# Kernel optimization log

Hardware: AMD Instinct MI355X
Metric: run time of the kernel (lower is better)

The kernel has to match this reference:

```python
import jax, jax.numpy as jnp
import numpy as np

DIM = 64; LAYERS = 3; NREL = 8; NB = 4
NNODE = 150000; NEDGE = 1000000; NSEDGE = 200000
BATCH = 1024; SEQ = 20; NPRED = 20; NITEM = 100000
TD = 2 * LAYERS * DIM  # 384
NEG = np.float32(-(2 ** 32) + 1)


def rgcn_layer(x, src, dst, et, basis, comp, root, bias):
    # basis decomposition: W_r = sum_b comp[r,b] * basis[b]  -> [R,d,d]
    W = jnp.einsum('rb,bde->rde', comp, basis)
    # transform all nodes by every relation once, then gather per edge
    xw = jnp.einsum('nd,rde->rne', x, W)          # [R,N,d]
    msgs = xw[et, src]                            # [E,d] gather (rate==1 gating)
    agg = jax.ops.segment_sum(msgs, dst, num_segments=x.shape[0])
    return agg + x @ root + bias


def tsal(seq, WQ, WK, WV):
    # hand-rolled causal self-attention, head_num=1; NOTE: softmax over axis=1
    # (query axis), faithful to F.softmax(output_tensor, 1) in the source.
    T = seq.shape[1]
    Q = seq @ WQ; K = seq @ WK; V = seq @ WV
    scores = jnp.einsum('bid,bjd->bij', Q, K) / jnp.sqrt(jnp.float32(T))
    tril = jnp.tril(jnp.ones((T, T), dtype=scores.dtype))
    scores = jnp.where(tril == 0, NEG, scores)
    attn = jax.nn.softmax(scores, axis=1)
    return jnp.einsum('bij,bjd->bid', attn, V)


def setup_inputs() -> dict:
    key = jax.random.key(0)
    ks = jax.random.split(key, 24)
    xav = lambda k, sh: jax.random.uniform(k, sh, jnp.float32, -1.0, 1.0) * np.float32(np.sqrt(6.0 / (sh[-1] + sh[-2])))
    node_emb = (jax.random.normal(ks[0], (NNODE, DIM), jnp.float32) / DIM).at[0].set(0.0)
    predict_w = (jax.random.normal(ks[1], (NITEM, TD), jnp.float32) / TD).at[0].set(0.0)
    predict_b = jnp.zeros((NITEM, 1), jnp.float32)
    sc_w = np.float32(np.sqrt(1.0 / DIM))
    basis = jax.random.normal(ks[2], (LAYERS, NB, DIM, DIM), jnp.float32) * sc_w
    comp = jax.random.normal(ks[3], (LAYERS, NREL, NB), jnp.float32) * np.float32(1.0 / NB)
    root = jax.random.normal(ks[4], (LAYERS, DIM, DIM), jnp.float32) * sc_w
    bias = jnp.zeros((LAYERS, DIM), jnp.float32)
    sbasis = jax.random.normal(ks[5], (LAYERS, NB, DIM, DIM), jnp.float32) * sc_w
    scomp = jax.random.normal(ks[6], (LAYERS, NREL, NB), jnp.float32) * np.float32(1.0 / NB)
    sroot = jax.random.normal(ks[7], (LAYERS, DIM, DIM), jnp.float32) * sc_w
    sbias = jnp.zeros((LAYERS, DIM), jnp.float32)
    WQ = xav(ks[8], (TD, TD)); WK = xav(ks[9], (TD, TD)); WV = xav(ks[10], (TD, TD))
    batch_users = jax.random.randint(ks[11], (BATCH,), 0, NNODE)
    batch_sequences = jax.random.randint(ks[12], (BATCH, SEQ), 0, NNODE)
    items_to_predict = jax.random.randint(ks[13], (BATCH, NPRED), 0, NITEM)
    edge_index = jax.random.randint(ks[14], (2, NEDGE), 0, NNODE)
    edge_type = jax.random.randint(ks[15], (NEDGE,), 0, NREL)
    node_no = jnp.arange(NNODE)
    short_edge_index = jax.random.randint(ks[16], (2, NSEDGE), 0, NNODE)
    short_edge_type = jax.random.randint(ks[17], (NSEDGE,), 0, NREL)
    return {"node_emb": node_emb, "predict_w": predict_w, "predict_b": predict_b,
            "basis": basis, "comp": comp, "root": root, "bias": bias,
            "sbasis": sbasis, "scomp": scomp, "sroot": sroot, "sbias": sbias,
            "WQ": WQ, "WK": WK, "WV": WV,
            "batch_users": batch_users, "batch_sequences": batch_sequences,
            "items_to_predict": items_to_predict, "edge_index": edge_index,
            "edge_type": edge_type, "node_no": node_no,
            "short_edge_index": short_edge_index, "short_edge_type": short_edge_type}


def reference(node_emb, predict_w, predict_b, basis, comp, root, bias,
              sbasis, scomp, sroot, sbias, WQ, WK, WV,
              batch_users, batch_sequences, items_to_predict,
              edge_index, edge_type, node_no, short_edge_index, short_edge_type):
    x = node_emb[node_no]
    states = []
    for l in range(LAYERS):
        x = jnp.tanh(rgcn_layer(x, edge_index[0], edge_index[1], edge_type,
                                basis[l], comp[l], root[l], bias[l]))
        states.append(x)
    for l in range(LAYERS):
        x = jnp.tanh(rgcn_layer(x, short_edge_index[0], short_edge_index[1], short_edge_type,
                                sbasis[l], scomp[l], sroot[l], sbias[l]))
        states.append(x)
    cs = jnp.concatenate(states, axis=1)             # [N, 2*LAYERS*DIM]
    user_emb = cs[batch_users]                       # [B, TD]
    item_embs_conv = cs[batch_sequences]             # [B, L, TD]
    item_embs = tsal(item_embs_conv, WQ, WK, WV)     # [B, L, TD]
    pe_w = predict_w[items_to_predict]               # [B, K, TD]
    pe_b = predict_b[items_to_predict][..., 0]       # [B, K]
    res = jnp.einsum('bkd,bd->bk', pe_w, user_emb) + pe_b      # baddbmm
    res = res + jnp.einsum('bld,bkd->bk', item_embs, pe_w)     # rel_score summed over L
    return (res, user_emb, item_embs_conv)
```

## Files before the change

kernel.cpp:

```cpp
#include <hip/hip_runtime.h>
#include <hip/hip_fp16.h>

typedef unsigned short u16;
typedef unsigned int   u32;

#define DIM    64
#define NREL   8
#define NB     4
#define NNODE  150000
#define NEDGE  1000000
#define NSEDGE 200000
#define BATCH  1024
#define SEQL   20
#define NPRED  20
#define TD     384

#define KC     576
#define KH     1152
#define KTILES 36
#define ROWD   580
#define NODES_PER_TILE 16

#define SCAN_CHUNK 2048

typedef float    f32x4 __attribute__((ext_vector_type(4)));
typedef _Float16 f16x8 __attribute__((ext_vector_type(8)));

__device__ __forceinline__ u32 packsplit(float v) {
    __half h = __float2half_rn(v);
    __half l = __float2half_rn(v - __half2float(h));
    __half2 p; p.x = h; p.y = l;
    u32 r;
    __builtin_memcpy(&r, &p, 4);
    return r;
}

__global__ __launch_bounds__(256) void wpackf_kernel(const float* __restrict__ comp,
                                                     const float* __restrict__ basis,
                                                     const float* __restrict__ root,
                                                     u32* __restrict__ Wf) {
    int idx = blockIdx.x * 256 + threadIdx.x;
    if (idx >= KTILES * 4 * 64) return;
    int l  = idx & 63;
    int f  = idx >> 6;
    int kt = f >> 2, ct = f & 3;
    int j  = ct * 16 + (l & 15);
    int kb = kt * 32 + (l >> 4) * 8;
    union { f16x8 v; u16 h[8]; } out;
#pragma unroll
    for (int u = 0; u < 8; ++u) {
        int c = (kb + u) >> 1;
        float v;
        if (c < 512) {
            int r = c >> 6, d = c & 63;
            v = comp[r * NB + 0] * basis[0 * 4096 + d * 64 + j]
              + comp[r * NB + 1] * basis[1 * 4096 + d * 64 + j]
              + comp[r * NB + 2] * basis[2 * 4096 + d * 64 + j]
              + comp[r * NB + 3] * basis[3 * 4096 + d * 64 + j];
        } else {
            int d = c & 63;
            v = root[d * 64 + j];
        }
        out.h[u] = (u16)__half_as_ushort(__float2half_rn(v));
    }
    *((f16x8*)Wf + idx) = out.v;
}


__global__ __launch_bounds__(256) void hist_kernel(const int* __restrict__ dst,
                                                   const int* __restrict__ typ,
                                                   int* __restrict__ cnt8, int E) {
    int i = blockIdx.x * 256 + threadIdx.x;
    const int stride = gridDim.x * 256;
    for (; i < E; i += stride) atomicAdd(&cnt8[dst[i] * NREL + typ[i]], 1);
}

__global__ __launch_bounds__(256) void blocksum_kernel(const int* __restrict__ cnt,
                                                       int* __restrict__ bsum, int N) {
    const int base = blockIdx.x * SCAN_CHUNK + threadIdx.x * 8;
    int s = 0;
#pragma unroll
    for (int u = 0; u < 8; ++u) {
        const int i = base + u;
        s += (i < N) ? cnt[i] : 0;
    }
#pragma unroll
    for (int o = 1; o < 64; o <<= 1) s += __shfl_xor(s, o, 64);
    __shared__ int ws[4];
    if ((threadIdx.x & 63) == 0) ws[threadIdx.x >> 6] = s;
    __syncthreads();
    if (threadIdx.x == 0) bsum[blockIdx.x] = ws[0] + ws[1] + ws[2] + ws[3];
}

__global__ __launch_bounds__(1024) void scanbsum_kernel(int* __restrict__ bsum, int B) {
    __shared__ int sh[1024];
    const int t = threadIdx.x;
    const int v = (t < B) ? bsum[t] : 0;
    sh[t] = v;
    __syncthreads();
    for (int o = 1; o < 1024; o <<= 1) {
        const int u = (t >= o) ? sh[t - o] : 0;
        __syncthreads();
        sh[t] += u;
        __syncthreads();
    }
    if (t < B) bsum[t] = sh[t] - v;
}

__global__ __launch_bounds__(256) void alloc2_kernel(const int* __restrict__ cnt,
                                                     const int* __restrict__ bsum,
                                                     int* __restrict__ rstart,
                                                     int* __restrict__ cursor, int N) {
    const int base = blockIdx.x * SCAN_CHUNK + threadIdx.x * 8;
    const int lane = threadIdx.x & 63;
    int c[8];
    int s = 0;
#pragma unroll
    for (int u = 0; u < 8; ++u) {
        const int i = base + u;
        c[u] = (i < N) ? cnt[i] : 0;
        s += c[u];
    }
    int v = s;
#pragma unroll
    for (int o = 1; o < 64; o <<= 1) {
        const int u2 = __shfl_up(v, o, 64);
        if (lane >= o) v += u2;
    }
    __shared__ int ws[4];
    if (lane == 63) ws[threadIdx.x >> 6] = v;
    __syncthreads();
    const int wv = threadIdx.x >> 6;
    int waveoff = 0;
#pragma unroll
    for (int k = 0; k < 4; ++k) waveoff += (k < wv) ? ws[k] : 0;
    int tbase = bsum[blockIdx.x] + waveoff + (v - s);
#pragma unroll
    for (int u = 0; u < 8; ++u) {
        const int i = base + u;
        if (i < N) {
            rstart[i] = tbase;
            cursor[i] = tbase;
            tbase += c[u];
        }
    }
}

__global__ __launch_bounds__(256) void scatter_kernel(const int* __restrict__ src,
                                                      const int* __restrict__ dst,
                                                      const int* __restrict__ typ,
                                                      int* __restrict__ cursor8,
                                                      u32* __restrict__ psrc, int E) {
    int i = blockIdx.x * 256 + threadIdx.x;
    const int stride = gridDim.x * 256;
    for (; i < E; i += stride) {
        const int slot = atomicAdd(&cursor8[dst[i] * NREL + typ[i]], 1);
        psrc[slot] = (u32)src[i];
    }
}

__global__ __launch_bounds__(512) void rgcn_mfma_kernel(const float* __restrict__ x,
                                                        const u32* __restrict__ Wf,
                                                        const float* __restrict__ bias,
                                                        const int* __restrict__ starts8,
                                                        const int* __restrict__ ends8,
                                                        const u32* __restrict__ psrc,
                                                        float* __restrict__ xout, int N) {
    __shared__ u32 Xl[NODES_PER_TILE * ROWD];
    const int lane = threadIdx.x & 63;
    const int w = threadIdx.x >> 6;
    const int NT = (N + NODES_PER_TILE - 1) / NODES_PER_TILE;
    const int l15 = lane & 15, g = lane >> 4;

    for (int tile = blockIdx.x; tile < NT; tile += gridDim.x) {
        const int base = tile * NODES_PER_TILE;
        for (int u = 0; u < 2; ++u) {
            const int row = w * 2 + u;
            const int n = base + row;
            if (n < N) {
                u32* Xrow = Xl + row * ROWD;
                const float xn = x[(size_t)n * 64 + lane];
                const int stl = starts8[n * NREL + (lane & 7)];
                const int enl = ends8[n * NREL + (lane & 7)];
                const int st0 = __shfl(stl, 0, 64);
                const int en7 = __shfl(enl, 7, 64);
                if (en7 - st0 <= 64) {
                    const u32 pk = (lane < en7 - st0) ? psrc[st0 + lane] : 0u;
#pragma unroll
                    for (int r = 0; r < NREL; ++r) {
                        const int st = __shfl(stl, r, 64) - st0;
                        const int en = __shfl(enl, r, 64) - st0;
                        float a0 = 0.f, a1 = 0.f;
                        int i = st;
                        for (; i + 1 < en; i += 2) {
                            const int s0 = (int)__shfl((int)pk, i, 64);
                            const int s1 = (int)__shfl((int)pk, i + 1, 64);
                            a0 += x[(size_t)s0 * 64 + lane];
                            a1 += x[(size_t)s1 * 64 + lane];
                        }
                        if (i < en) {
                            const int s0 = (int)__shfl((int)pk, i, 64);
                            a0 += x[(size_t)s0 * 64 + lane];
                        }
                        Xrow[r * 64 + lane] = packsplit(a0 + a1);
                    }
                } else {
#pragma unroll 1
                    for (int r = 0; r < NREL; ++r) {
                        const int st = __shfl(stl, r, 64);
                        const int en = __shfl(enl, r, 64);
                        float acc = 0.f;
                        for (int i2 = st; i2 < en; i2 += 64) {
                            int mm = en - i2; if (mm > 64) mm = 64;
                            int pkc = (lane < mm) ? (int)psrc[i2 + lane] : 0;
                            for (int t = 0; t < mm; ++t) {
                                const int s = __shfl(pkc, t, 64);
                                acc += x[(size_t)s * 64 + lane];
                            }
                        }
                        Xrow[r * 64 + lane] = packsplit(acc);
                    }
                }
                Xrow[512 + lane] = packsplit(xn);
            }
        }
        __syncthreads();
        if (w < 4) {
            const int ct = w;
            const u32* Arow = Xl + l15 * ROWD + g * 4;
            const f16x8* Bf = (const f16x8*)Wf + ct * 64 + lane;
            f32x4 acc = {0.f, 0.f, 0.f, 0.f};
#pragma unroll 4
            for (int kt = 0; kt < KTILES; ++kt) {
                f16x8 a = *(const f16x8*)(Arow + kt * 16);
                f16x8 b = Bf[kt * 256];
                acc = __builtin_amdgcn_mfma_f32_16x16x32_f16(a, b, acc, 0, 0, 0);
            }
            const int col = ct * 16 + l15;
            const float bc = bias[col];
#pragma unroll
            for (int q = 0; q < 4; ++q) {
                const int n = base + g * 4 + q;
                if (n < N) xout[(size_t)n * 64 + col] = tanhf(acc[q] + bc);
            }
        }
        __syncthreads();
    }
}

__global__ __launch_bounds__(256) void post_kernel(const float* __restrict__ xc,
                                                   const int* __restrict__ users,
                                                   const int* __restrict__ seqs,
                                                   float* __restrict__ msum,
                                                   float* __restrict__ out_user,
                                                   float* __restrict__ out_seq, int l) {
    const int lane = threadIdx.x & 63;
    int wave = blockIdx.x * 4 + (threadIdx.x >> 6);
    const int nw = gridDim.x * 4;
    for (int p = wave; p < BATCH * SEQL; p += nw) {
        const int idx = seqs[p];
        out_seq[(size_t)p * TD + l * 64 + lane] = xc[(size_t)idx * 64 + lane];
    }
    for (int b = wave; b < BATCH; b += nw) {
        out_user[(size_t)b * TD + l * 64 + lane] = xc[(size_t)users[b] * 64 + lane];
        float m = 0.f;
        for (int t = 0; t < SEQL; ++t)
            m += xc[(size_t)seqs[b * SEQL + t] * 64 + lane];
        msum[(size_t)b * TD + l * 64 + lane] = m;
    }
}

__global__ __launch_bounds__(384) void final_kernel(const float* __restrict__ msum,
                                                    const float* __restrict__ user_f32,
                                                    const float* __restrict__ WV,
                                                    const float* __restrict__ pw,
                                                    const float* __restrict__ pb,
                                                    const int* __restrict__ items,
                                                    float* __restrict__ out_res) {
    __shared__ float ms[TD];
    __shared__ float uL[TD];
    const int b = blockIdx.x;
    const int o = threadIdx.x;
    ms[o] = msum[(size_t)b * TD + o];
    __syncthreads();
    float sv = 0.f;
#pragma unroll 4
    for (int d = 0; d < TD; ++d) sv += ms[d] * WV[d * TD + o];
    uL[o] = user_f32[(size_t)b * TD + o] + sv;
    __syncthreads();
    const int w = threadIdx.x >> 6, lane = threadIdx.x & 63;
    for (int k = w; k < NPRED; k += 6) {
        const int item = items[b * NPRED + k];
        const float* pwr = pw + (size_t)item * TD;
        float a = 0.f;
#pragma unroll
        for (int d = lane; d < TD; d += 64) a += pwr[d] * uL[d];
#pragma unroll
        for (int off = 32; off; off >>= 1) a += __shfl_down(a, off, 64);
        if (lane == 0) out_res[b * NPRED + k] = a + pb[item];
    }
}

extern "C" void kernel_launch(void* const* d_in, const int* in_sizes, int n_in,
                              void* d_out, int out_size, void* d_ws, size_t ws_size,
                              hipStream_t stream) {
    const float* node_emb  = (const float*)d_in[0];
    const float* predict_w = (const float*)d_in[1];
    const float* predict_b = (const float*)d_in[2];
    const float* basis     = (const float*)d_in[3];
    const float* comp      = (const float*)d_in[4];
    const float* root      = (const float*)d_in[5];
    const float* bias      = (const float*)d_in[6];
    const float* sbasis    = (const float*)d_in[7];
    const float* scomp     = (const float*)d_in[8];
    const float* sroot     = (const float*)d_in[9];
    const float* sbias     = (const float*)d_in[10];
    const float* WV        = (const float*)d_in[13];
    const int* users       = (const int*)d_in[14];
    const int* seqs        = (const int*)d_in[15];
    const int* items       = (const int*)d_in[16];
    const int* eidx        = (const int*)d_in[17];
    const int* etyp        = (const int*)d_in[18];
    const int* seidx       = (const int*)d_in[20];
    const int* setyp       = (const int*)d_in[21];

    float* xA    = (float*)d_ws;
    float* xB    = xA + (size_t)NNODE * 64;
    u32*   Wf    = (u32*)(xB + (size_t)NNODE * 64);
    float* msum  = (float*)(Wf + KTILES * 4 * 64 * 4);
    int*   cnt8  = (int*)(msum + (size_t)BATCH * TD);
    int*   stB   = cnt8 + (size_t)NNODE * NREL;
    int*   enB   = stB  + (size_t)NNODE * NREL;
    int*   stS   = enB  + (size_t)NNODE * NREL;
    int*   enS   = stS  + (size_t)NNODE * NREL;
    int*   bsum  = enS  + (size_t)NNODE * NREL;
    u32*   pB    = (u32*)(bsum + 1024);
    u32*   pS    = pB + NEDGE;

    float* out      = (float*)d_out;
    float* out_res  = out;
    float* out_user = out + BATCH * NPRED;
    float* out_seq  = out_user + (size_t)BATCH * TD;

    const int N8 = NNODE * NREL;
    const int NBLK = (N8 + SCAN_CHUNK - 1) / SCAN_CHUNK;
    hipMemsetAsync(cnt8, 0, (size_t)N8 * sizeof(int), stream);
    hist_kernel<<<2048, 256, 0, stream>>>(eidx + NEDGE, etyp, cnt8, NEDGE);
    blocksum_kernel<<<NBLK, 256, 0, stream>>>(cnt8, bsum, N8);
    scanbsum_kernel<<<1, 1024, 0, stream>>>(bsum, NBLK);
    alloc2_kernel<<<NBLK, 256, 0, stream>>>(cnt8, bsum, stB, enB, N8);
    scatter_kernel<<<2048, 256, 0, stream>>>(eidx, eidx + NEDGE, etyp, enB, pB, NEDGE);
    hipMemsetAsync(cnt8, 0, (size_t)N8 * sizeof(int), stream);
    hist_kernel<<<784, 256, 0, stream>>>(seidx + NSEDGE, setyp, cnt8, NSEDGE);
    blocksum_kernel<<<NBLK, 256, 0, stream>>>(cnt8, bsum, N8);
    scanbsum_kernel<<<1, 1024, 0, stream>>>(bsum, NBLK);
    alloc2_kernel<<<NBLK, 256, 0, stream>>>(cnt8, bsum, stS, enS, N8);
    scatter_kernel<<<784, 256, 0, stream>>>(seidx, seidx + NSEDGE, setyp, enS, pS, NSEDGE);

    const float* xc = node_emb;
    for (int l = 0; l < 6; ++l) {
        const float *bs, *cp, *rt, *bi;
        const int *rs, *re;
        const u32* pk;
        if (l < 3) {
            bs = basis  + (size_t)l * NB * DIM * DIM;
            cp = comp   + l * NREL * NB;
            rt = root   + l * DIM * DIM;
            bi = bias   + l * DIM;
            rs = stB; re = enB; pk = pB;
        } else {
            const int m = l - 3;
            bs = sbasis + (size_t)m * NB * DIM * DIM;
            cp = scomp  + m * NREL * NB;
            rt = sroot  + m * DIM * DIM;
            bi = sbias  + m * DIM;
            rs = stS; re = enS; pk = pS;
        }
        float* xg = (l & 1) ? xB : xA;
        wpackf_kernel<<<36, 256, 0, stream>>>(cp, bs, rt, Wf);
        rgcn_mfma_kernel<<<2048, 512, 0, stream>>>(xc, Wf, bi, rs, re, pk, xg, NNODE);
        post_kernel<<<320, 256, 0, stream>>>(xg, users, seqs, msum, out_user, out_seq, l);
        xc = xg;
    }

    final_kernel<<<BATCH, 384, 0, stream>>>(msum, out_user, WV, predict_w, predict_b,
                                            items, out_res);
}
```

Measured before the change: 1.169 ms.

## Pack relation type into edge source index and accumulate per-relation in LDS

The scatter kernel now stores the edge type in the upper bits of each packed source index. The aggregation loop can then walk all of a node's edges in one flat pass, four gathers at a time, and add each row into a per-relation float slot in shared memory instead of running eight separate per-relation loops. Per-node metadata, self features and the first 64 packed indices for both nodes are loaded up front to overlap the latency. In exchange, accumulation goes through LDS read-modify-write, and the packing assumes node ids fit in 18 bits.

```diff
diff --git a/kernel.cpp b/kernel.cpp
--- a/kernel.cpp
+++ b/kernel.cpp
@@ -155,7 +155,7 @@
     const int stride = gridDim.x * 256;
     for (; i < E; i += stride) {
         const int slot = atomicAdd(&cursor8[dst[i] * NREL + typ[i]], 1);
-        psrc[slot] = (u32)src[i];
+        psrc[slot] = (u32)src[i] | ((u32)typ[i] << 18);
     }
 }
 
@@ -174,54 +174,69 @@
 
     for (int tile = blockIdx.x; tile < NT; tile += gridDim.x) {
         const int base = tile * NODES_PER_TILE;
+        const int n0 = base + w * 2;
+        int nst0 = 0, nen0 = 0, nst1 = 0, nen1 = 0;
+        float xn0 = 0.f, xn1 = 0.f;
+        if (n0 < N) {
+            nst0 = starts8[n0 * NREL];
+            nen0 = ends8[n0 * NREL + 7];
+            xn0  = x[(size_t)n0 * 64 + lane];
+        }
+        if (n0 + 1 < N) {
+            nst1 = starts8[(n0 + 1) * NREL];
+            nen1 = ends8[(n0 + 1) * NREL + 7];
+            xn1  = x[(size_t)(n0 + 1) * 64 + lane];
+        }
+        u32 pk0 = 0, pk1 = 0;
+        if (lane < nen0 - nst0) pk0 = psrc[nst0 + lane];
+        if (lane < nen1 - nst1) pk1 = psrc[nst1 + lane];
+#pragma unroll
         for (int u = 0; u < 2; ++u) {
-            const int row = w * 2 + u;
-            const int n = base + row;
+            const int n = n0 + u;
             if (n < N) {
+                const int row = w * 2 + u;
                 u32* Xrow = Xl + row * ROWD;
-                const float xn = x[(size_t)n * 64 + lane];
-                const int stl = starts8[n * NREL + (lane & 7)];
-                const int enl = ends8[n * NREL + (lane & 7)];
-                const int st0 = __shfl(stl, 0, 64);
-                const int en7 = __shfl(enl, 7, 64);
-                if (en7 - st0 <= 64) {
-                    const u32 pk = (lane < en7 - st0) ? psrc[st0 + lane] : 0u;
-#pragma unroll
-                    for (int r = 0; r < NREL; ++r) {
-                        const int st = __shfl(stl, r, 64) - st0;
-                        const int en = __shfl(enl, r, 64) - st0;
-                        float a0 = 0.f, a1 = 0.f;
-                        int i = st;
-                        for (; i + 1 < en; i += 2) {
-                            const int s0 = (int)__shfl((int)pk, i, 64);
-                            const int s1 = (int)__shfl((int)pk, i + 1, 64);
-                            a0 += x[(size_t)s0 * 64 + lane];
-                            a1 += x[(size_t)s1 * 64 + lane];
+                float* XrowF = (float*)Xrow;
+#pragma unroll
+                for (int r = 0; r < NREL; ++r) XrowF[r * 64 + lane] = 0.f;
+                const u32 pk = u ? pk1 : pk0;
+                const int nst = u ? nst1 : nst0;
+                const int nen = u ? nen1 : nen0;
+                const int tot = nen - nst;
+                const int cw = tot > 64 ? 64 : tot;
+                int t = 0;
+                for (; t + 4 <= cw; t += 4) {
+                    const u32 p0 = __shfl(pk, t + 0, 64);
+                    const u32 p1 = __shfl(pk, t + 1, 64);
+                    const u32 p2 = __shfl(pk, t + 2, 64);
+                    const u32 p3 = __shfl(pk, t + 3, 64);
+                    const float v0 = x[(size_t)(p0 & 0x3FFFFu) * 64 + lane];
+                    const float v1 = x[(size_t)(p1 & 0x3FFFFu) * 64 + lane];
+                    const float v2 = x[(size_t)(p2 & 0x3FFFFu) * 64 + lane];
+                    const float v3 = x[(size_t)(p3 & 0x3FFFFu) * 64 + lane];
+                    XrowF[(p0 >> 18) * 64 + lane] += v0;
+                    XrowF[(p1 >> 18) * 64 + lane] += v1;
+                    XrowF[(p2 >> 18) * 64 + lane] += v2;
+                    XrowF[(p3 >> 18) * 64 + lane] += v3;
+                }
+                for (; t < cw; ++t) {
+                    const u32 p = __shfl(pk, t, 64);
+                    XrowF[(p >> 18) * 64 + lane] += x[(size_t)(p & 0x3FFFFu) * 64 + lane];
+                }
+                if (tot > 64) {
+                    for (int i2 = nst + 64; i2 < nen; i2 += 64) {
+                        int mm = nen - i2; if (mm > 64) mm = 64;
+                        const u32 pkc = (lane < mm) ? psrc[i2 + lane] : 0u;
+                        for (int tt = 0; tt < mm; ++tt) {
+                            const u32 p = __shfl(pkc, tt, 64);
+                            XrowF[(p >> 18) * 64 + lane] += x[(size_t)(p & 0x3FFFFu) * 64 + lane];
                         }
-                        if (i < en) {
-                            const int s0 = (int)__shfl((int)pk, i, 64);
-                            a0 += x[(size_t)s0 * 64 + lane];
-                        }
-                        Xrow[r * 64 + lane] = packsplit(a0 + a1);
-                    }
-                } else {
-#pragma unroll 1
-                    for (int r = 0; r < NREL; ++r) {
-                        const int st = __shfl(stl, r, 64);
-                        const int en = __shfl(enl, r, 64);
-                        float acc = 0.f;
-                        for (int i2 = st; i2 < en; i2 += 64) {
-                            int mm = en - i2; if (mm > 64) mm = 64;
-                            int pkc = (lane < mm) ? (int)psrc[i2 + lane] : 0;
-                            for (int t = 0; t < mm; ++t) {
-                                const int s = __shfl(pkc, t, 64);
-                                acc += x[(size_t)s * 64 + lane];
-                            }
-                        }
-                        Xrow[r * 64 + lane] = packsplit(acc);
                     }
                 }
-                Xrow[512 + lane] = packsplit(xn);
+#pragma unroll
+                for (int r = 0; r < NREL; ++r)
+                    Xrow[r * 64 + lane] = packsplit(XrowF[r * 64 + lane]);
+                Xrow[512 + lane] = packsplit(u ? xn1 : xn0);
             }
         }
         __syncthreads();
```

Result: faster. 1.045 ms (-10.6%).
